# Optimization experiments

Hardware: AMD Instinct MI355X
Metric: run time of the kernel (lower is better)

## Reference

```python
import jax, jax.numpy as jnp
import numpy as np

VAR_EPS = 1e-05


def setup_inputs() -> dict:
    key = jax.random.key(0)
    k1, k2 = jax.random.split(key)
    B, T = 1024, 16384
    pred = jax.random.normal(k1, (B, T), dtype=jnp.float32)
    target = jax.random.normal(k2, (B, T), dtype=jnp.float32)
    return {"pred": pred, "target": target}


def reference(pred, target):
    # Per-row Pearson correlation, vectorized over the batch dimension.
    T = pred.shape[1]
    mp = jnp.mean(pred, axis=1, keepdims=True)
    mt = jnp.mean(target, axis=1, keepdims=True)
    cp = pred - mp                      # [B, T] centered
    ct = target - mt
    sp = jnp.sum(cp * cp, axis=1)       # [B] sum of squares
    st = jnp.sum(ct * ct, axis=1)
    num = jnp.sum(cp * ct, axis=1)      # [B] covariance numerator
    # torch.var uses unbiased estimator (correction=1)
    var_p = sp / (T - 1)
    var_t = st / (T - 1)
    denom = jnp.sqrt(sp * st)
    safe_denom = jnp.where(denom > 0, denom, 1.0)
    corr = num / safe_denom
    valid = (var_p > VAR_EPS) & (var_t > VAR_EPS) & (denom > 0) & ~jnp.isnan(corr)
    per_row = jnp.where(valid, 1.0 - corr, 1.0)
    return jnp.mean(per_row)
```

## Files before the change

### kernel.cpp

```cpp
#include <hip/hip_runtime.h>

#define T_LEN 16384
#define VAR_EPS 1e-5f

__global__ __launch_bounds__(256) void pearson_row_kernel(
    const float* __restrict__ pred, const float* __restrict__ target,
    float* __restrict__ row_loss)
{
    const int row = blockIdx.x;
    const int tid = threadIdx.x;
    const float4* __restrict__ p4 =
        (const float4*)(pred + (size_t)row * T_LEN);
    const float4* __restrict__ t4 =
        (const float4*)(target + (size_t)row * T_LEN);

    float sp = 0.f, st = 0.f, spp = 0.f, stt = 0.f, spt = 0.f;

    #pragma unroll 4
    for (int i = tid; i < T_LEN / 4; i += 256) {
        float4 a = p4[i];
        float4 b = t4[i];
        sp  += a.x + a.y + a.z + a.w;
        st  += b.x + b.y + b.z + b.w;
        spp += a.x * a.x + a.y * a.y + a.z * a.z + a.w * a.w;
        stt += b.x * b.x + b.y * b.y + b.z * b.z + b.w * b.w;
        spt += a.x * b.x + a.y * b.y + a.z * b.z + a.w * b.w;
    }

    #pragma unroll
    for (int off = 32; off > 0; off >>= 1) {
        sp  += __shfl_down(sp,  off);
        st  += __shfl_down(st,  off);
        spp += __shfl_down(spp, off);
        stt += __shfl_down(stt, off);
        spt += __shfl_down(spt, off);
    }

    __shared__ float ws[4][5];
    const int lane = tid & 63;
    const int wave = tid >> 6;
    if (lane == 0) {
        ws[wave][0] = sp;  ws[wave][1] = st;  ws[wave][2] = spp;
        ws[wave][3] = stt; ws[wave][4] = spt;
    }
    __syncthreads();

    if (tid == 0) {
        float S_p  = ws[0][0] + ws[1][0] + ws[2][0] + ws[3][0];
        float S_t  = ws[0][1] + ws[1][1] + ws[2][1] + ws[3][1];
        float S_pp = ws[0][2] + ws[1][2] + ws[2][2] + ws[3][2];
        float S_tt = ws[0][3] + ws[1][3] + ws[2][3] + ws[3][3];
        float S_pt = ws[0][4] + ws[1][4] + ws[2][4] + ws[3][4];

        const float T   = (float)T_LEN;
        const float inv = 1.0f / T;
        float cp2 = S_pp - S_p * S_p * inv;
        float ct2 = S_tt - S_t * S_t * inv;
        float num = S_pt - S_p * S_t * inv;

        float var_p = cp2 / (T - 1.0f);
        float var_t = ct2 / (T - 1.0f);
        float denom = sqrtf(cp2 * ct2);
        float safe  = (denom > 0.0f) ? denom : 1.0f;
        float corr  = num / safe;
        bool valid = (var_p > VAR_EPS) && (var_t > VAR_EPS) &&
                     (denom > 0.0f) && !isnan(corr);
        row_loss[row] = valid ? (1.0f - corr) : 1.0f;
    }
}

__global__ __launch_bounds__(256) void reduce_mean_kernel(
    const float* __restrict__ row_loss, float* __restrict__ out, int B)
{
    const int tid = threadIdx.x;
    float s = 0.f;
    for (int i = tid; i < B; i += 256) s += row_loss[i];

    #pragma unroll
    for (int off = 32; off > 0; off >>= 1) s += __shfl_down(s, off);

    __shared__ float ws[4];
    if ((tid & 63) == 0) ws[tid >> 6] = s;
    __syncthreads();
    if (tid == 0)
        out[0] = (ws[0] + ws[1] + ws[2] + ws[3]) / (float)B;
}

extern "C" void kernel_launch(void* const* d_in, const int* in_sizes, int n_in,
                              void* d_out, int out_size, void* d_ws, size_t ws_size,
                              hipStream_t stream) {
    const float* pred   = (const float*)d_in[0];
    const float* target = (const float*)d_in[1];
    float* out = (float*)d_out;
    float* row_loss = (float*)d_ws;

    const int B = in_sizes[0] / T_LEN;

    pearson_row_kernel<<<B, 256, 0, stream>>>(pred, target, row_loss);
    reduce_mean_kernel<<<1, 256, 0, stream>>>(row_loss, out, B);
}
```

Baseline: 145.0 us.

## Fuse row reduction and mean via atomicAdd, widen blocks, front-load all loads

Drops the second reduce_mean kernel: each row block now scales its loss by 1/B and atomically adds it into the output, which is zeroed with a memset beforehand. Blocks grow to 512 threads, and the strided loop becomes two fully unrolled halves that issue eight float4 loads up front to raise memory-level parallelism. This saves one kernel launch and the row_loss round trip. In exchange it adds a memset, 1024 contended atomics on a single address, and a summation order that is no longer deterministic.

Result: no change. 144.9 us (-0.1%).

```diff
diff --git a/kernel.cpp b/kernel.cpp
--- a/kernel.cpp
+++ b/kernel.cpp
@@ -3,9 +3,9 @@
 #define T_LEN 16384
 #define VAR_EPS 1e-5f
 
-__global__ __launch_bounds__(256) void pearson_row_kernel(
+__global__ __launch_bounds__(512) void pearson_row_kernel(
     const float* __restrict__ pred, const float* __restrict__ target,
-    float* __restrict__ row_loss)
+    float* __restrict__ out, float inv_B)
 {
     const int row = blockIdx.x;
     const int tid = threadIdx.x;
@@ -16,15 +16,34 @@
 
     float sp = 0.f, st = 0.f, spp = 0.f, stt = 0.f, spt = 0.f;
 
-    #pragma unroll 4
-    for (int i = tid; i < T_LEN / 4; i += 256) {
-        float4 a = p4[i];
-        float4 b = t4[i];
-        sp  += a.x + a.y + a.z + a.w;
-        st  += b.x + b.y + b.z + b.w;
-        spp += a.x * a.x + a.y * a.y + a.z * a.z + a.w * a.w;
-        stt += b.x * b.x + b.y * b.y + b.z * b.z + b.w * b.w;
-        spt += a.x * b.x + a.y * b.y + a.z * b.z + a.w * b.w;
+    #pragma unroll
+    for (int half = 0; half < 2; ++half) {
+        const int i0 = tid + half * 2048;
+        float4 a0 = p4[i0];
+        float4 a1 = p4[i0 + 512];
+        float4 a2 = p4[i0 + 1024];
+        float4 a3 = p4[i0 + 1536];
+        float4 b0 = t4[i0];
+        float4 b1 = t4[i0 + 512];
+        float4 b2 = t4[i0 + 1024];
+        float4 b3 = t4[i0 + 1536];
+
+        sp  += (a0.x + a0.y + a0.z + a0.w) + (a1.x + a1.y + a1.z + a1.w)
+             + (a2.x + a2.y + a2.z + a2.w) + (a3.x + a3.y + a3.z + a3.w);
+        st  += (b0.x + b0.y + b0.z + b0.w) + (b1.x + b1.y + b1.z + b1.w)
+             + (b2.x + b2.y + b2.z + b2.w) + (b3.x + b3.y + b3.z + b3.w);
+        spp += a0.x*a0.x + a0.y*a0.y + a0.z*a0.z + a0.w*a0.w
+             + a1.x*a1.x + a1.y*a1.y + a1.z*a1.z + a1.w*a1.w
+             + a2.x*a2.x + a2.y*a2.y + a2.z*a2.z + a2.w*a2.w
+             + a3.x*a3.x + a3.y*a3.y + a3.z*a3.z + a3.w*a3.w;
+        stt += b0.x*b0.x + b0.y*b0.y + b0.z*b0.z + b0.w*b0.w
+             + b1.x*b1.x + b1.y*b1.y + b1.z*b1.z + b1.w*b1.w
+             + b2.x*b2.x + b2.y*b2.y + b2.z*b2.z + b2.w*b2.w
+             + b3.x*b3.x + b3.y*b3.y + b3.z*b3.z + b3.w*b3.w;
+        spt += a0.x*b0.x + a0.y*b0.y + a0.z*b0.z + a0.w*b0.w
+             + a1.x*b1.x + a1.y*b1.y + a1.z*b1.z + a1.w*b1.w
+             + a2.x*b2.x + a2.y*b2.y + a2.z*b2.z + a2.w*b2.w
+             + a3.x*b3.x + a3.y*b3.y + a3.z*b3.z + a3.w*b3.w;
     }
 
     #pragma unroll
@@ -36,7 +55,7 @@
         spt += __shfl_down(spt, off);
     }
 
-    __shared__ float ws[4][5];
+    __shared__ float ws[8][5];
     const int lane = tid & 63;
     const int wave = tid >> 6;
     if (lane == 0) {
@@ -46,11 +65,12 @@
     __syncthreads();
 
     if (tid == 0) {
-        float S_p  = ws[0][0] + ws[1][0] + ws[2][0] + ws[3][0];
-        float S_t  = ws[0][1] + ws[1][1] + ws[2][1] + ws[3][1];
-        float S_pp = ws[0][2] + ws[1][2] + ws[2][2] + ws[3][2];
-        float S_tt = ws[0][3] + ws[1][3] + ws[2][3] + ws[3][3];
-        float S_pt = ws[0][4] + ws[1][4] + ws[2][4] + ws[3][4];
+        float S_p = 0.f, S_t = 0.f, S_pp = 0.f, S_tt = 0.f, S_pt = 0.f;
+        #pragma unroll
+        for (int w = 0; w < 8; ++w) {
+            S_p  += ws[w][0]; S_t  += ws[w][1]; S_pp += ws[w][2];
+            S_tt += ws[w][3]; S_pt += ws[w][4];
+        }
 
         const float T   = (float)T_LEN;
         const float inv = 1.0f / T;
@@ -65,25 +85,9 @@
         float corr  = num / safe;
         bool valid = (var_p > VAR_EPS) && (var_t > VAR_EPS) &&
                      (denom > 0.0f) && !isnan(corr);
-        row_loss[row] = valid ? (1.0f - corr) : 1.0f;
+        float loss = valid ? (1.0f - corr) : 1.0f;
+        atomicAdd(out, loss * inv_B);
     }
-}
-
-__global__ __launch_bounds__(256) void reduce_mean_kernel(
-    const float* __restrict__ row_loss, float* __restrict__ out, int B)
-{
-    const int tid = threadIdx.x;
-    float s = 0.f;
-    for (int i = tid; i < B; i += 256) s += row_loss[i];
-
-    #pragma unroll
-    for (int off = 32; off > 0; off >>= 1) s += __shfl_down(s, off);
-
-    __shared__ float ws[4];
-    if ((tid & 63) == 0) ws[tid >> 6] = s;
-    __syncthreads();
-    if (tid == 0)
-        out[0] = (ws[0] + ws[1] + ws[2] + ws[3]) / (float)B;
 }
 
 extern "C" void kernel_launch(void* const* d_in, const int* in_sizes, int n_in,
@@ -92,10 +96,9 @@
     const float* pred   = (const float*)d_in[0];
     const float* target = (const float*)d_in[1];
     float* out = (float*)d_out;
-    float* row_loss = (float*)d_ws;
 
     const int B = in_sizes[0] / T_LEN;
 
-    pearson_row_kernel<<<B, 256, 0, stream>>>(pred, target, row_loss);
-    reduce_mean_kernel<<<1, 256, 0, stream>>>(row_loss, out, B);
+    hipMemsetAsync(out, 0, sizeof(float), stream);
+    pearson_row_kernel<<<B, 512, 0, stream>>>(pred, target, out, 1.0f / (float)B);
 }
```
